# Kernel optimization log

Hardware: AMD Instinct MI355X
Metric: run time of the kernel (lower is better)

Reference implementation:

```python
import jax, jax.numpy as jnp
import numpy as np

B, S, D, W, P = 32, 512, 768, 256, 1024


def setup_inputs() -> dict:
    key = jax.random.key(0)
    k_h, k_len, k_pair, k_w1, k_w2 = jax.random.split(key, 5)
    h = jax.random.normal(k_h, (B, S, D), dtype=jnp.float32)
    # ragged word spans: each word covers 1 or 2 contiguous subwords; total <= S
    word_len = jax.random.randint(k_len, (B, W), 1, 3, dtype=jnp.int32)  # in {1,2}
    word_start = jnp.concatenate(
        [jnp.zeros((B, 1), jnp.int32), jnp.cumsum(word_len, axis=1)[:, :-1]], axis=1
    )
    # word-index pairs per configuration; -1 means "use zero embedding"
    pair_idx = jax.random.randint(k_pair, (B, P, 2), 0, W + 1, dtype=jnp.int32) - 1
    w1 = jax.random.normal(k_w1, (2 * D, 300), dtype=jnp.float32) * 0.02
    b1 = jnp.zeros((300,), jnp.float32)
    w2 = jax.random.normal(k_w2, (300, 4), dtype=jnp.float32) * 0.02
    b2 = jnp.zeros((4,), jnp.float32)
    return {"h": h, "w1": w1, "b1": b1, "w2": w2, "b2": b2,
            "word_start": word_start, "word_len": word_len, "pair_idx": pair_idx}


def reference(h, w1, b1, w2, b2, word_start, word_len, pair_idx):
    # --- mean-pool subword embeddings per word via prefix sums (segment mean) ---
    csum = jnp.cumsum(h, axis=1)                                   # [B,S,D]
    csum = jnp.concatenate([jnp.zeros_like(csum[:, :1]), csum], 1)  # [B,S+1,D]
    end = word_start + word_len                                     # [B,W]
    seg_sum = (jnp.take_along_axis(csum, end[:, :, None], axis=1)
               - jnp.take_along_axis(csum, word_start[:, :, None], axis=1))
    word_emb = seg_sum / word_len[:, :, None].astype(h.dtype)       # [B,W,D]
    # --- per-pair gather with -1 -> zero vector ---
    valid = (pair_idx >= 0)                                         # [B,P,2]
    idx = jnp.maximum(pair_idx, 0).reshape(h.shape[0], -1)          # [B,2P]
    emb = jnp.take_along_axis(word_emb, idx[:, :, None], axis=1)    # [B,2P,D]
    emb = emb.reshape(pair_idx.shape[0], pair_idx.shape[1], 2, -1)
    emb = jnp.where(valid[..., None], emb, jnp.zeros((), h.dtype))
    mlp_input = emb.reshape(-1, 2 * h.shape[-1])                    # [B*P, 2D]
    # --- tiny MLP + softmax (dropout is identity in eval) ---
    x = jnp.tanh(mlp_input @ w1 + b1)
    return jax.nn.softmax(x @ w2 + b2, axis=-1)                     # [B*P, 4]
```

## Files before the change

kernel.cpp:

```cpp
#include <hip/hip_runtime.h>
#include <cstddef>
#include <cstdint>

#define Bb   32
#define Ss   512
#define Dd   768
#define Ww   256
#define Pp   1024
#define NH   300
#define SLOT1 320
#define NPAD 640
#define Mm   (Bb * Ww)
#define ZROW 8192
#define ZOFF (ZROW * NPAD)
#define PBUF ((Mm + 1) * NPAD)
#define KH   384

typedef __attribute__((ext_vector_type(8))) short bf16x8;
typedef __attribute__((ext_vector_type(4))) float f32x4;

#define GPTR(p) ((const __attribute__((address_space(1))) void*)(p))
#define LPTR(p) ((__attribute__((address_space(3))) void*)(p))

__device__ __forceinline__ unsigned short f2bf(float x) {
    unsigned u = __builtin_bit_cast(unsigned, x);
    u += 0x7fffu + ((u >> 16) & 1u);
    return (unsigned short)(u >> 16);
}
__device__ __forceinline__ float bf2f(unsigned short u) {
    return __builtin_bit_cast(float, (unsigned)u << 16);
}
__device__ __forceinline__ unsigned pk2(float a, float b) {
    return (unsigned)f2bf(a) | ((unsigned)f2bf(b) << 16);
}
__device__ __forceinline__ float fast_tanh(float x) {
    x = fminf(fmaxf(x, -15.0f), 15.0f);
    float e = __expf(2.0f * x);
    return 1.0f - 2.0f * __builtin_amdgcn_rcpf(e + 1.0f);
}

__global__ __launch_bounds__(256) void prep_kernel(
    const float* __restrict__ w1, unsigned short* __restrict__ bmatT,
    unsigned short* __restrict__ proj)
{
    const int gid    = blockIdx.x * 256 + threadIdx.x;
    const int stride = 512 * 256;

    for (int u = gid; u < Dd * NPAD; u += stride) {
        const int k = u / NPAD;
        const int n = u - k * NPAD;
        float v = 0.0f;
        if (n < NH)                            v = w1[(size_t)k * NH + n];
        else if (n >= SLOT1 && n < SLOT1 + NH) v = w1[(size_t)(Dd + k) * NH + (n - SLOT1)];
        bmatT[(size_t)n * Dd + k] = f2bf(v);
    }

    if (gid < NPAD / 4) {
        *(ushort4*)(proj + ZOFF + gid * 4)        = make_ushort4(0, 0, 0, 0);
        *(ushort4*)(proj + PBUF + ZOFF + gid * 4) = make_ushort4(0, 0, 0, 0);
    }
}

__global__ __launch_bounds__(256) void gemm_kernel(
    const float* __restrict__ h,
    const int* __restrict__ word_start, const int* __restrict__ word_len,
    const unsigned short* __restrict__ bmatT,
    unsigned short* __restrict__ proj)
{
    __shared__ bf16x8 Al[2][4][128];
    __shared__ bf16x8 Bl[2][4][128];

    const int bid = blockIdx.x;
    const int t   = threadIdx.x;

    const int swz   = (bid & 7) * 80 + (bid >> 3);
    const int kh    = swz / 320;
    const int tIdx  = swz - kh * 320;
    const int mBase = (tIdx / 5) * 128;
    const int nBase = (tIdx % 5) * 128;
    const int kOff  = kh * KH;

    const int srow_s = t >> 3;
    const int chunk  = t & 7;
    const float* hpA[4];
    const float* hpB[4];
#pragma unroll
    for (int p = 0; p < 4; ++p) {
        const int arow = mBase + srow_s + p * 32;
        const int s0   = word_start[arow];
        const int len  = word_len[arow];
        const float* base = h + (size_t)(arow >> 8) * (Ss * Dd)
                              + (size_t)s0 * Dd + kOff + chunk * 4;
        hpA[p] = base;
        hpB[p] = base + (size_t)(len - 1) * Dd;
    }
    const int aByte = (chunk >> 1) * 2048 + srow_s * 16 + (chunk & 1) * 8;

    const unsigned short* srcB =
        bmatT + (size_t)(nBase + (t & 127)) * Dd + kOff + ((t >> 7) << 3);
    char* ldsB = (char*)&Bl[0][0][0] + t * 16;

    const int lane = t & 63;
    const int w    = t >> 6;
    const int wr   = w >> 1;
    const int wc   = w & 1;
    const int fr   = lane & 15;
    const int kb   = lane >> 4;

    f32x4 acc[4][4];
#pragma unroll
    for (int i = 0; i < 4; ++i)
#pragma unroll
        for (int j = 0; j < 4; ++j)
#pragma unroll
            for (int r = 0; r < 4; ++r) acc[i][j][r] = 0.0f;

    float4 hx[4], hy[4];

#define HLOAD(k0_)                                                        \
    {                                                                     \
        _Pragma("unroll")                                                 \
        for (int p = 0; p < 4; ++p) {                                     \
            hx[p] = *(const float4*)(hpA[p] + (k0_));                     \
            hy[p] = *(const float4*)(hpB[p] + (k0_));                     \
        }                                                                 \
    }

#define POOLW(c)                                                          \
    {                                                                     \
        _Pragma("unroll")                                                 \
        for (int p = 0; p < 4; ++p) {                                     \
            uint2 o;                                                      \
            o.x = pk2((hx[p].x + hy[p].x) * 0.5f,                         \
                      (hx[p].y + hy[p].y) * 0.5f);                        \
            o.y = pk2((hx[p].z + hy[p].z) * 0.5f,                         \
                      (hx[p].w + hy[p].w) * 0.5f);                        \
            *(uint2*)((char*)&Al[0][0][0] + (c) * 8192 + aByte            \
                      + p * (32 * 16)) = o;                               \
        }                                                                 \
    }

#define STAGEB(c, off)                                                                         \
    __builtin_amdgcn_global_load_lds(GPTR(srcB + (off)),      LPTR(ldsB + (c) * 8192),        16, 0, 0); \
    __builtin_amdgcn_global_load_lds(GPTR(srcB + (off) + 16), LPTR(ldsB + (c) * 8192 + 4096), 16, 0, 0)

#define COMPUTE(c)                                                                             \
    {                                                                                          \
        bf16x8 a[4], b[4];                                                                     \
        _Pragma("unroll")                                                                      \
        for (int mi = 0; mi < 4; ++mi) a[mi] = Al[c][kb][wr * 64 + mi * 16 + fr];              \
        _Pragma("unroll")                                                                      \
        for (int ni = 0; ni < 4; ++ni) b[ni] = Bl[c][kb][wc * 64 + ni * 16 + fr];              \
        _Pragma("unroll")                                                                      \
        for (int mi = 0; mi < 4; ++mi)                                                         \
            _Pragma("unroll")                                                                  \
            for (int ni = 0; ni < 4; ++ni)                                                     \
                acc[mi][ni] = __builtin_amdgcn_mfma_f32_16x16x32_bf16(a[mi], b[ni], acc[mi][ni], 0, 0, 0); \
    }

    HLOAD(0);
    STAGEB(0, 0);
    POOLW(0);
    __syncthreads();

    int cur = 0;
    for (int k0 = 32; k0 < KH; k0 += 32) {
        HLOAD(k0);
        STAGEB(cur ^ 1, k0);
        COMPUTE(cur);
        POOLW(cur ^ 1);
        __syncthreads();
        cur ^= 1;
    }
    COMPUTE(cur);
#undef HLOAD
#undef POOLW
#undef STAGEB
#undef COMPUTE

    unsigned short* projh = proj + (size_t)kh * PBUF;
    const int r0 = mBase + wr * 64 + kb * 4;
    const int c0 = nBase + wc * 64 + fr;
#pragma unroll
    for (int mi = 0; mi < 4; ++mi)
#pragma unroll
        for (int ni = 0; ni < 4; ++ni)
#pragma unroll
            for (int r = 0; r < 4; ++r)
                projh[(size_t)(r0 + mi * 16 + r) * NPAD + c0 + ni * 16] = f2bf(acc[mi][ni][r]);
}

__global__ __launch_bounds__(256) void mlp_kernel(
    const unsigned short* __restrict__ proj,
    const float* __restrict__ b1, const float* __restrict__ w2,
    const float* __restrict__ b2, const int* __restrict__ pair_idx,
    float* __restrict__ out)
{
    __shared__ float red[4][64][17];

    const int wv   = threadIdx.x >> 6;
    const int wave = blockIdx.x * 4 + wv;
    const int lane = threadIdx.x & 63;
    const int wid0 = wave * 4;
    const int b    = wid0 >> 10;
    const int rbase = b * Ww * NPAD;
    const unsigned short* proj1 = proj + PBUF;

    const int4 piA = *(const int4*)(pair_idx + wid0 * 2);
    const int4 piB = *(const int4*)(pair_idx + wid0 * 2 + 4);
    const int idx[8] = {piA.x, piA.y, piA.z, piA.w, piB.x, piB.y, piB.z, piB.w};

    int off0[4], off1[4];
#pragma unroll
    for (int p = 0; p < 4; ++p) {
        const int i0 = idx[p * 2], i1 = idx[p * 2 + 1];
        off0[p] = (i0 >= 0) ? rbase + i0 * NPAD : ZOFF;
        off1[p] = ((i1 >= 0) ? rbase + i1 * NPAD : ZOFF) + SLOT1;
    }

    unsigned short g0a[4][5], g0b[4][5], g1a[4][5], g1b[4][5];
#pragma unroll
    for (int p = 0; p < 4; ++p)
#pragma unroll
        for (int it = 0; it < 5; ++it) {
            const int j = lane + it * 64;
            g0a[p][it] = proj [(size_t)off0[p] + j];
            g0b[p][it] = proj1[(size_t)off0[p] + j];
            g1a[p][it] = proj [(size_t)off1[p] + j];
            g1b[p][it] = proj1[(size_t)off1[p] + j];
        }

    float acc[4][4];
#pragma unroll
    for (int p = 0; p < 4; ++p)
#pragma unroll
        for (int c = 0; c < 4; ++c) acc[p][c] = 0.0f;

#pragma unroll
    for (int it = 0; it < 5; ++it) {
        const int j  = lane + it * 64;
        const bool ok = (j < NH);
        const float bj = ok ? b1[j] : 0.0f;
        float4 wv4 = make_float4(0.f, 0.f, 0.f, 0.f);
        if (ok) wv4 = *(const float4*)(w2 + (size_t)j * 4);
#pragma unroll
        for (int p = 0; p < 4; ++p) {
            const float v = bj + (bf2f(g0a[p][it]) + bf2f(g0b[p][it]))
                               + (bf2f(g1a[p][it]) + bf2f(g1b[p][it]));
            const float x = ok ? fast_tanh(v) : 0.0f;
            acc[p][0] = fmaf(x, wv4.x, acc[p][0]);
            acc[p][1] = fmaf(x, wv4.y, acc[p][1]);
            acc[p][2] = fmaf(x, wv4.z, acc[p][2]);
            acc[p][3] = fmaf(x, wv4.w, acc[p][3]);
        }
    }

#pragma unroll
    for (int p = 0; p < 4; ++p)
#pragma unroll
        for (int c = 0; c < 4; ++c)
            red[wv][lane][p * 4 + c] = acc[p][c];
    __syncthreads();

    const int o = lane >> 2;
    const int g = lane & 3;
    float v = 0.0f;
#pragma unroll
    for (int i = 0; i < 16; ++i)
        v += red[wv][g * 16 + i][o];
    v += __shfl_xor(v, 1, 64);
    v += __shfl_xor(v, 2, 64);

    const int c = o & 3;
    const float l = v + b2[c];
    float mx = fmaxf(l, __shfl_xor(l, 4, 64));
    mx = fmaxf(mx, __shfl_xor(mx, 8, 64));
    const float e = __expf(l - mx);
    float s = e + __shfl_xor(e, 4, 64);
    s += __shfl_xor(s, 8, 64);
    const float r = e * __builtin_amdgcn_rcpf(s);
    if (g == 0)
        out[(size_t)(wid0 + (o >> 2)) * 4 + c] = r;
}

extern "C" void kernel_launch(void* const* d_in, const int* in_sizes, int n_in,
                              void* d_out, int out_size, void* d_ws, size_t ws_size,
                              hipStream_t stream)
{
    const float* h          = (const float*)d_in[0];
    const float* w1         = (const float*)d_in[1];
    const float* b1         = (const float*)d_in[2];
    const float* w2         = (const float*)d_in[3];
    const float* b2         = (const float*)d_in[4];
    const int*   word_start = (const int*)d_in[5];
    const int*   word_len   = (const int*)d_in[6];
    const int*   pair_idx   = (const int*)d_in[7];
    float*       out        = (float*)d_out;

    unsigned short* proj  = (unsigned short*)d_ws;
    unsigned short* bmatT = (unsigned short*)((char*)d_ws + 20975616);

    prep_kernel<<<dim3(512),  dim3(256), 0, stream>>>(w1, bmatT, proj);
    gemm_kernel<<<dim3(640),  dim3(256), 0, stream>>>(h, word_start, word_len, bmatT, proj);
    mlp_kernel <<<dim3(2048), dim3(256), 0, stream>>>(proj, b1, w2, b2, pair_idx, out);
}
```

Measured before the change: 50.28 us.

## Deepen GEMM prefetch to two stages with triple-buffered B tiles

The fused pool+GEMM main loop now prefetches two K-steps ahead. B tiles are triple-buffered in LDS, and the h activation loads are double-buffered in registers. The loop is fully unrolled over the 12 K-steps. The plain __syncthreads is replaced by a barrier that waits only on LDS counters, so outstanding global loads can stay in flight across barriers. This aims to hide global memory latency behind the MFMA work, at the cost of more registers and LDS. It relies on the compiler's vmcnt waits for the h registers to also cover the earlier global_load_lds into B.

```diff
diff --git a/kernel.cpp b/kernel.cpp
--- a/kernel.cpp
+++ b/kernel.cpp
@@ -15,6 +15,7 @@
 #define ZOFF (ZROW * NPAD)
 #define PBUF ((Mm + 1) * NPAD)
 #define KH   384
+#define NST  12
 
 typedef __attribute__((ext_vector_type(8))) short bf16x8;
 typedef __attribute__((ext_vector_type(4))) float f32x4;
@@ -68,7 +69,7 @@
     unsigned short* __restrict__ proj)
 {
     __shared__ bf16x8 Al[2][4][128];
-    __shared__ bf16x8 Bl[2][4][128];
+    __shared__ bf16x8 Bl[3][4][128];
 
     const int bid = blockIdx.x;
     const int t   = threadIdx.x;
@@ -115,26 +116,26 @@
 #pragma unroll
             for (int r = 0; r < 4; ++r) acc[i][j][r] = 0.0f;
 
-    float4 hx[4], hy[4];
-
-#define HLOAD(k0_)                                                        \
+    float4 hx[2][4], hy[2][4];
+
+#define HLOADS(s, k0_)                                                    \
     {                                                                     \
         _Pragma("unroll")                                                 \
         for (int p = 0; p < 4; ++p) {                                     \
-            hx[p] = *(const float4*)(hpA[p] + (k0_));                     \
-            hy[p] = *(const float4*)(hpB[p] + (k0_));                     \
+            hx[s][p] = *(const float4*)(hpA[p] + (k0_));                  \
+            hy[s][p] = *(const float4*)(hpB[p] + (k0_));                  \
         }                                                                 \
     }
 
-#define POOLW(c)                                                          \
+#define POOLW(c, s)                                                       \
     {                                                                     \
         _Pragma("unroll")                                                 \
         for (int p = 0; p < 4; ++p) {                                     \
             uint2 o;                                                      \
-            o.x = pk2((hx[p].x + hy[p].x) * 0.5f,                         \
-                      (hx[p].y + hy[p].y) * 0.5f);                        \
-            o.y = pk2((hx[p].z + hy[p].z) * 0.5f,                         \
-                      (hx[p].w + hy[p].w) * 0.5f);                        \
+            o.x = pk2((hx[s][p].x + hy[s][p].x) * 0.5f,                   \
+                      (hx[s][p].y + hy[s][p].y) * 0.5f);                  \
+            o.y = pk2((hx[s][p].z + hy[s][p].z) * 0.5f,                   \
+                      (hx[s][p].w + hy[s][p].w) * 0.5f);                  \
             *(uint2*)((char*)&Al[0][0][0] + (c) * 8192 + aByte            \
                       + p * (32 * 16)) = o;                               \
         }                                                                 \
@@ -144,13 +145,13 @@
     __builtin_amdgcn_global_load_lds(GPTR(srcB + (off)),      LPTR(ldsB + (c) * 8192),        16, 0, 0); \
     __builtin_amdgcn_global_load_lds(GPTR(srcB + (off) + 16), LPTR(ldsB + (c) * 8192 + 4096), 16, 0, 0)
 
-#define COMPUTE(c)                                                                             \
+#define COMPUTE(ab, bb)                                                                        \
     {                                                                                          \
         bf16x8 a[4], b[4];                                                                     \
         _Pragma("unroll")                                                                      \
-        for (int mi = 0; mi < 4; ++mi) a[mi] = Al[c][kb][wr * 64 + mi * 16 + fr];              \
+        for (int mi = 0; mi < 4; ++mi) a[mi] = Al[ab][kb][wr * 64 + mi * 16 + fr];             \
         _Pragma("unroll")                                                                      \
-        for (int ni = 0; ni < 4; ++ni) b[ni] = Bl[c][kb][wc * 64 + ni * 16 + fr];              \
+        for (int ni = 0; ni < 4; ++ni) b[ni] = Bl[bb][kb][wc * 64 + ni * 16 + fr];             \
         _Pragma("unroll")                                                                      \
         for (int mi = 0; mi < 4; ++mi)                                                         \
             _Pragma("unroll")                                                                  \
@@ -158,25 +159,34 @@
                 acc[mi][ni] = __builtin_amdgcn_mfma_f32_16x16x32_bf16(a[mi], b[ni], acc[mi][ni], 0, 0, 0); \
     }
 
-    HLOAD(0);
-    STAGEB(0, 0);
-    POOLW(0);
-    __syncthreads();
-
-    int cur = 0;
-    for (int k0 = 32; k0 < KH; k0 += 32) {
-        HLOAD(k0);
-        STAGEB(cur ^ 1, k0);
-        COMPUTE(cur);
-        POOLW(cur ^ 1);
-        __syncthreads();
-        cur ^= 1;
-    }
-    COMPUTE(cur);
-#undef HLOAD
+#define LBAR()                                                            \
+    __builtin_amdgcn_sched_barrier(0);                                    \
+    asm volatile("s_waitcnt lgkmcnt(0)" ::: "memory");                    \
+    __builtin_amdgcn_s_barrier();                                         \
+    __builtin_amdgcn_sched_barrier(0)
+
+    STAGEB(0, 0);  HLOADS(0, 0);
+    STAGEB(1, 32); HLOADS(1, 32);
+    POOLW(0, 0);
+    LBAR();
+
+#pragma unroll
+    for (int k = 0; k < NST; ++k) {
+        if (k < NST - 2) {
+            STAGEB((k + 2) % 3, (k + 2) * 32);
+            HLOADS(k % 2, (k + 2) * 32);
+        }
+        COMPUTE(k % 2, k % 3);
+        if (k < NST - 1) {
+            POOLW((k + 1) % 2, (k + 1) % 2);
+            LBAR();
+        }
+    }
+#undef HLOADS
 #undef POOLW
 #undef STAGEB
 #undef COMPUTE
+#undef LBAR
 
     unsigned short* projh = proj + (size_t)kh * PBUF;
     const int r0 = mBase + wr * 64 + kb * 4;
```

After: 54.32 us. 1.08x slower.

## Drop split-K in projection GEMM and read a single partial buffer in MLP

Applied to the files above, without the earlier changes.

The GEMM no longer splits K into two halves written to separate bf16 partial buffers. Each block now covers the full K=768 reduction, and the grid shrinks from 640 to 320 blocks. The MLP kernel gathers one projection buffer instead of two and adds fewer terms, which cuts partial-buffer writes and gather traffic. The cost is half the blocks, each running a K loop twice as long, which lowers parallelism and may hurt load balance across CUs.

```diff
diff --git a/kernel.cpp b/kernel.cpp
--- a/kernel.cpp
+++ b/kernel.cpp
@@ -13,8 +13,6 @@
 #define Mm   (Bb * Ww)
 #define ZROW 8192
 #define ZOFF (ZROW * NPAD)
-#define PBUF ((Mm + 1) * NPAD)
-#define KH   384
 
 typedef __attribute__((ext_vector_type(8))) short bf16x8;
 typedef __attribute__((ext_vector_type(4))) float f32x4;
@@ -55,10 +53,8 @@
         bmatT[(size_t)n * Dd + k] = f2bf(v);
     }
 
-    if (gid < NPAD / 4) {
-        *(ushort4*)(proj + ZOFF + gid * 4)        = make_ushort4(0, 0, 0, 0);
-        *(ushort4*)(proj + PBUF + ZOFF + gid * 4) = make_ushort4(0, 0, 0, 0);
-    }
+    if (gid < NPAD / 4)
+        *(ushort4*)(proj + ZOFF + gid * 4) = make_ushort4(0, 0, 0, 0);
 }
 
 __global__ __launch_bounds__(256) void gemm_kernel(
@@ -73,12 +69,9 @@
     const int bid = blockIdx.x;
     const int t   = threadIdx.x;
 
-    const int swz   = (bid & 7) * 80 + (bid >> 3);
-    const int kh    = swz / 320;
-    const int tIdx  = swz - kh * 320;
-    const int mBase = (tIdx / 5) * 128;
-    const int nBase = (tIdx % 5) * 128;
-    const int kOff  = kh * KH;
+    const int swz   = (bid & 7) * 40 + (bid >> 3);
+    const int mBase = (swz / 5) * 128;
+    const int nBase = (swz % 5) * 128;
 
     const int srow_s = t >> 3;
     const int chunk  = t & 7;
@@ -90,14 +83,14 @@
         const int s0   = word_start[arow];
         const int len  = word_len[arow];
         const float* base = h + (size_t)(arow >> 8) * (Ss * Dd)
-                              + (size_t)s0 * Dd + kOff + chunk * 4;
+                              + (size_t)s0 * Dd + chunk * 4;
         hpA[p] = base;
         hpB[p] = base + (size_t)(len - 1) * Dd;
     }
     const int aByte = (chunk >> 1) * 2048 + srow_s * 16 + (chunk & 1) * 8;
 
     const unsigned short* srcB =
-        bmatT + (size_t)(nBase + (t & 127)) * Dd + kOff + ((t >> 7) << 3);
+        bmatT + (size_t)(nBase + (t & 127)) * Dd + ((t >> 7) << 3);
     char* ldsB = (char*)&Bl[0][0][0] + t * 16;
 
     const int lane = t & 63;
@@ -164,7 +157,7 @@
     __syncthreads();
 
     int cur = 0;
-    for (int k0 = 32; k0 < KH; k0 += 32) {
+    for (int k0 = 32; k0 < Dd; k0 += 32) {
         HLOAD(k0);
         STAGEB(cur ^ 1, k0);
         COMPUTE(cur);
@@ -178,7 +171,6 @@
 #undef STAGEB
 #undef COMPUTE
 
-    unsigned short* projh = proj + (size_t)kh * PBUF;
     const int r0 = mBase + wr * 64 + kb * 4;
     const int c0 = nBase + wc * 64 + fr;
 #pragma unroll
@@ -187,7 +179,7 @@
         for (int ni = 0; ni < 4; ++ni)
 #pragma unroll
             for (int r = 0; r < 4; ++r)
-                projh[(size_t)(r0 + mi * 16 + r) * NPAD + c0 + ni * 16] = f2bf(acc[mi][ni][r]);
+                proj[(size_t)(r0 + mi * 16 + r) * NPAD + c0 + ni * 16] = f2bf(acc[mi][ni][r]);
 }
 
 __global__ __launch_bounds__(256) void mlp_kernel(
@@ -204,7 +196,6 @@
     const int wid0 = wave * 4;
     const int b    = wid0 >> 10;
     const int rbase = b * Ww * NPAD;
-    const unsigned short* proj1 = proj + PBUF;
 
     const int4 piA = *(const int4*)(pair_idx + wid0 * 2);
     const int4 piB = *(const int4*)(pair_idx + wid0 * 2 + 4);
@@ -218,16 +209,14 @@
         off1[p] = ((i1 >= 0) ? rbase + i1 * NPAD : ZOFF) + SLOT1;
     }
 
-    unsigned short g0a[4][5], g0b[4][5], g1a[4][5], g1b[4][5];
+    unsigned short g0[4][5], g1[4][5];
 #pragma unroll
     for (int p = 0; p < 4; ++p)
 #pragma unroll
         for (int it = 0; it < 5; ++it) {
             const int j = lane + it * 64;
-            g0a[p][it] = proj [(size_t)off0[p] + j];
-            g0b[p][it] = proj1[(size_t)off0[p] + j];
-            g1a[p][it] = proj [(size_t)off1[p] + j];
-            g1b[p][it] = proj1[(size_t)off1[p] + j];
+            g0[p][it] = proj[(size_t)off0[p] + j];
+            g1[p][it] = proj[(size_t)off1[p] + j];
         }
 
     float acc[4][4];
@@ -245,8 +234,7 @@
         if (ok) wv4 = *(const float4*)(w2 + (size_t)j * 4);
 #pragma unroll
         for (int p = 0; p < 4; ++p) {
-            const float v = bj + (bf2f(g0a[p][it]) + bf2f(g0b[p][it]))
-                               + (bf2f(g1a[p][it]) + bf2f(g1b[p][it]));
+            const float v = bj + bf2f(g0[p][it]) + bf2f(g1[p][it]);
             const float x = ok ? fast_tanh(v) : 0.0f;
             acc[p][0] = fmaf(x, wv4.x, acc[p][0]);
             acc[p][1] = fmaf(x, wv4.y, acc[p][1]);
@@ -298,9 +286,9 @@
     float*       out        = (float*)d_out;
 
     unsigned short* proj  = (unsigned short*)d_ws;
-    unsigned short* bmatT = (unsigned short*)((char*)d_ws + 20975616);
+    unsigned short* bmatT = (unsigned short*)((char*)d_ws + 16777216);
 
     prep_kernel<<<dim3(512),  dim3(256), 0, stream>>>(w1, bmatT, proj);
-    gemm_kernel<<<dim3(640),  dim3(256), 0, stream>>>(h, word_start, word_len, bmatT, proj);
+    gemm_kernel<<<dim3(320),  dim3(256), 0, stream>>>(h, word_start, word_len, bmatT, proj);
     mlp_kernel <<<dim3(2048), dim3(256), 0, stream>>>(proj, b1, w2, b2, pair_idx, out);
 }
```

Result: slower. 53.79 us (+7.0%).
